# Kernel tuning notes

Hardware: AMD Instinct MI355X
Metric: run time of the kernel (lower is better)

The kernel has to match this reference:

```python
import jax, jax.numpy as jnp
import numpy as np

N = 20000      # nodes
E = 200000     # edges
IN = 128       # in_feat
OUT = 128      # out_feat
NB = 8         # num_bases
SI = IN // NB  # submat_in = 16
SO = OUT // NB # submat_out = 16
R = 230        # num_rels
T = 365        # total_times


def setup_inputs() -> dict:
    key = jax.random.key(0)
    ks = jax.random.split(key, 11)
    h = jax.random.normal(ks[0], (N, IN), jnp.float32)
    edge_norm = jax.random.uniform(ks[1], (E, 1), jnp.float32)
    node_norm = jax.random.uniform(ks[2], (N, 1), jnp.float32)
    weight = jax.random.normal(ks[3], (R, NB * SI * SO), jnp.float32) * 0.05
    h_bias = jnp.zeros((OUT,), jnp.float32)
    loop_weight = jax.random.normal(ks[4], (IN, OUT), jnp.float32) * 0.05
    time_embed = jax.random.normal(ks[5], (T, IN), jnp.float32) * 0.05
    edge_src = jax.random.randint(ks[6], (E,), 0, N)
    edge_dst = jax.random.randint(ks[7], (E,), 0, N)
    edge_type = jax.random.randint(ks[8], (E,), 0, R)
    time_idx = jax.random.randint(ks[9], (N,), 0, T)
    return dict(h=h, edge_norm=edge_norm, node_norm=node_norm, weight=weight,
                h_bias=h_bias, loop_weight=loop_weight, time_embed=time_embed,
                edge_src=edge_src, edge_dst=edge_dst, edge_type=edge_type,
                time_idx=time_idx)


def reference(h, edge_norm, node_norm, weight, h_bias, loop_weight, time_embed,
              edge_src, edge_dst, edge_type, time_idx):
    # self-loop message
    loop_message = h @ loop_weight                              # [N, OUT]
    # msg_func: per-edge relation weight gather + block-diagonal bmm
    W_e = weight[edge_type].reshape(-1, NB, SI, SO)             # [E, NB, SI, SO]
    src = h[edge_src].reshape(-1, NB, SI)                       # [E, NB, SI]
    msg = jnp.einsum('ebi,ebio->ebo', src, W_e).reshape(-1, OUT)  # [E, OUT]
    msg = msg * edge_norm
    # fn.sum aggregation over destination nodes
    agg = jax.ops.segment_sum(msg, edge_dst, num_segments=N)    # [N, OUT]
    # apply_func: scale by node norm, then bias + self loop + activation
    node_repr = agg * node_norm
    node_repr = node_repr + h_bias + loop_message
    node_repr = jax.nn.relu(node_repr)
    # get_time_embedding: per-node time embedding gather
    time_embedding = time_embed[time_idx]                       # [N, IN]
    return node_repr, time_embedding
```

## Files before the change

### kernel.cpp

```cpp
#include <hip/hip_runtime.h>

#define N 20000
#define E 200000
#define IN 128
#define OUT 128
#define NB 8
#define SI 16
#define SO 16
#define R 230
#define T 365

#define NSH 8
#define NSEG (R * NSH)

#define ALLOC_BLOCKS 86
#define SL_BLOCKS 625
#define TE_BLOCKS 313
#define GRID2 (ALLOC_BLOCKS + SL_BLOCKS + TE_BLOCKS)

__device__ float  g_W_t[(size_t)R * NB * SO * SI];
__device__ ushort g_msg[(size_t)E * OUT];
__device__ float  g_sl[(size_t)N * OUT];
__device__ int    g_cnt_d[N];
__device__ int    g_off_d[N];
__device__ int    g_cur_d[N];
__device__ int    g_cnt_r[NSEG * 16];
__device__ int    g_cur_r[NSEG * 16];
__device__ int    g_eid_r[E];
__device__ int    g_total_d;
__device__ int    g_total_r;

__device__ __forceinline__ ushort f2bf(float f) {
    unsigned u = __float_as_uint(f);
    return (ushort)((u + 0x7fffu + ((u >> 16) & 1u)) >> 16);
}
__device__ __forceinline__ float bflo(unsigned m) { return __uint_as_float(m << 16); }
__device__ __forceinline__ float bfhi(unsigned m) { return __uint_as_float(m & 0xffff0000u); }

__global__ __launch_bounds__(256) void hist_kernel(
        const float* __restrict__ weight,
        const int* __restrict__ edge_dst,
        const int* __restrict__ edge_type) {
    __shared__ int lh[NSEG];
    const int tid  = threadIdx.x;
    const int gtid = blockIdx.x * 256 + tid;
    const int GSZ  = gridDim.x * 256;

    for (int t = gtid; t < R * NB * SI * SO; t += GSZ) {
        int r  = t >> 11;
        int b  = (t >> 8) & 7;
        int ol = (t >> 4) & 15;
        int i  = t & 15;
        g_W_t[t] = weight[(size_t)r * 2048 + b * 256 + i * 16 + ol];
    }
    for (int j = tid; j < NSEG; j += 256) lh[j] = 0;
    __syncthreads();
    for (int e = gtid; e < E; e += GSZ) {
        atomicAdd(&g_cnt_d[edge_dst[e]], 1);
        atomicAdd(&lh[edge_type[e] * NSH + (e & (NSH - 1))], 1);
    }
    __syncthreads();
    for (int j = tid; j < NSEG; j += 256)
        if (lh[j]) atomicAdd(&g_cnt_r[j * 16], lh[j]);
}

__global__ __launch_bounds__(256) void alloc_aux_kernel(
        const float* __restrict__ h,
        const float* __restrict__ loop_weight,
        const float* __restrict__ h_bias,
        const float* __restrict__ time_embed,
        const int* __restrict__ time_idx,
        float* __restrict__ out) {
    __shared__ __attribute__((aligned(16))) float hsm[32 * 132];
    const int bid = blockIdx.x;
    const int tid = threadIdx.x;

    if (bid < ALLOC_BLOCKS) {
        const int idx  = bid * 256 + tid;
        const int lane = tid & 63;
        const int NPAD = 20032;
        if (idx < NPAD) {
            int c = (idx < N) ? g_cnt_d[idx] : 0;
            int x = c;
            for (int d = 1; d < 64; d <<= 1) {
                int y = __shfl_up(x, d);
                if (lane >= d) x += y;
            }
            int base = 0;
            if (lane == 63) base = atomicAdd(&g_total_d, x);
            base = __shfl(base, 63);
            if (idx < N) {
                int off = base + x - c;
                g_off_d[idx] = off;
                g_cur_d[idx] = off;
            }
        } else {
            int j = idx - NPAD;
            if (j < 1856) {
                int c = (j < NSEG) ? g_cnt_r[j * 16] : 0;
                int x = c;
                for (int d = 1; d < 64; d <<= 1) {
                    int y = __shfl_up(x, d);
                    if (lane >= d) x += y;
                }
                int base = 0;
                if (lane == 63) base = atomicAdd(&g_total_r, x);
                base = __shfl(base, 63);
                if (j < NSEG) g_cur_r[j * 16] = base + x - c;
            }
        }
        return;
    }

    if (bid < ALLOC_BLOCKS + SL_BLOCKS) {
        const int a   = bid - ALLOC_BLOCKS;
        const int nb0 = a * 32;

        for (int k = tid; k < 32 * IN; k += 256) {
            int nl = k >> 7;
            int i  = k & 127;
            hsm[nl * 132 + i] = h[(size_t)(nb0 + nl) * IN + i];
        }
        __syncthreads();

        const int q    = tid & 63;
        const int wave = tid >> 6;
        const int nb   = wave * 8;
        const float2* lw2 = reinterpret_cast<const float2*>(loop_weight);
        float sL[8], sH[8];
#pragma unroll
        for (int j = 0; j < 8; ++j) { sL[j] = 0.f; sH[j] = 0.f; }
        for (int i0 = 0; i0 < IN; i0 += 4) {
            float2 w0 = lw2[(size_t)(i0 + 0) * 64 + q];
            float2 w1 = lw2[(size_t)(i0 + 1) * 64 + q];
            float2 w2 = lw2[(size_t)(i0 + 2) * 64 + q];
            float2 w3 = lw2[(size_t)(i0 + 3) * 64 + q];
#pragma unroll
            for (int j = 0; j < 8; ++j) {
                float4 v = *reinterpret_cast<const float4*>(
                    &hsm[(nb + j) * 132 + i0]);
                sL[j] = fmaf(v.x, w0.x, sL[j]); sL[j] = fmaf(v.y, w1.x, sL[j]);
                sL[j] = fmaf(v.z, w2.x, sL[j]); sL[j] = fmaf(v.w, w3.x, sL[j]);
                sH[j] = fmaf(v.x, w0.y, sH[j]); sH[j] = fmaf(v.y, w1.y, sH[j]);
                sH[j] = fmaf(v.z, w2.y, sH[j]); sH[j] = fmaf(v.w, w3.y, sH[j]);
            }
        }
        const float2 bias = reinterpret_cast<const float2*>(h_bias)[q];
        float2* sl2 = reinterpret_cast<float2*>(g_sl);
#pragma unroll
        for (int j = 0; j < 8; ++j) {
            float2 v; v.x = sL[j] + bias.x; v.y = sH[j] + bias.y;
            sl2[(size_t)(nb0 + nb + j) * 64 + q] = v;
        }
        return;
    }

    const int c    = bid - ALLOC_BLOCKS - SL_BLOCKS;
    const int row  = tid >> 2;
    const int part = tid & 3;
    const int n    = c * 64 + row;
    if (n < N) {
        const float4* src = reinterpret_cast<const float4*>(
            time_embed + (size_t)time_idx[n] * IN);
        float4* dst = reinterpret_cast<float4*>(
            out + (size_t)N * OUT + (size_t)n * IN);
#pragma unroll
        for (int j = 0; j < 8; ++j)
            dst[part * 8 + j] = src[part * 8 + j];
    }
}

__global__ void scatter_kernel(const int* __restrict__ edge_type) {
    int e = blockIdx.x * blockDim.x + threadIdx.x;
    if (e < E) {
        int seg = edge_type[e] * NSH + (e & (NSH - 1));
        int pr = atomicAdd(&g_cur_r[seg * 16], 1);
        g_eid_r[pr] = e;
    }
}

__global__ __launch_bounds__(256) void msg_kernel(
        const float* __restrict__ h,
        const float* __restrict__ edge_norm,
        const int* __restrict__ edge_src,
        const int* __restrict__ edge_dst,
        const int* __restrict__ edge_type) {
    __shared__ __attribute__((aligned(16))) float hsm[32 * 132];
    __shared__ int   ssrc[32], stype[32], spos[32];
    __shared__ float snorm[32];

    const int tid = threadIdx.x;
    const int lo  = blockIdx.x * 32;

    if (tid < 32) {
        int e = g_eid_r[lo + tid];
        ssrc[tid]  = edge_src[e];
        stype[tid] = edge_type[e];
        snorm[tid] = edge_norm[e];
        spos[tid]  = atomicAdd(&g_cur_d[edge_dst[e]], 1);
    }
    __syncthreads();

    {
        const int row = tid >> 3;
        const int c0  = (tid & 7) * 4;
        const float* hp = h + (size_t)ssrc[row] * IN;
        float* dst = &hsm[row * 132];
#pragma unroll
        for (int j = 0; j < 4; ++j) {
            float4 v = *reinterpret_cast<const float4*>(hp + c0 + 32 * j);
            *reinterpret_cast<float4*>(dst + c0 + 32 * j) = v;
        }
    }
    __syncthreads();

    const int slot = tid >> 7;
    const int o    = tid & 127;
    const int b    = o >> 4;
    const int ol   = o & 15;

#define MSG_BODY(K, W0, W1, W2, W3)                                          \
    {                                                                        \
        const float* hrow = &hsm[(K) * 132 + b * 16];                        \
        float4 h0 = *reinterpret_cast<const float4*>(hrow);                  \
        float4 h1 = *reinterpret_cast<const float4*>(hrow + 4);              \
        float4 h2 = *reinterpret_cast<const float4*>(hrow + 8);              \
        float4 h3 = *reinterpret_cast<const float4*>(hrow + 12);             \
        float m0 = 0.f, m1 = 0.f;                                            \
        m0 = fmaf(h0.x, W0.x, m0); m0 = fmaf(h0.y, W0.y, m0);                \
        m0 = fmaf(h0.z, W0.z, m0); m0 = fmaf(h0.w, W0.w, m0);                \
        m1 = fmaf(h1.x, W1.x, m1); m1 = fmaf(h1.y, W1.y, m1);                \
        m1 = fmaf(h1.z, W1.z, m1); m1 = fmaf(h1.w, W1.w, m1);                \
        m0 = fmaf(h2.x, W2.x, m0); m0 = fmaf(h2.y, W2.y, m0);                \
        m0 = fmaf(h2.z, W2.z, m0); m0 = fmaf(h2.w, W2.w, m0);                \
        m1 = fmaf(h3.x, W3.x, m1); m1 = fmaf(h3.y, W3.y, m1);                \
        m1 = fmaf(h3.z, W3.z, m1); m1 = fmaf(h3.w, W3.w, m1);                \
        __builtin_nontemporal_store(f2bf(snorm[K] * (m0 + m1)),              \
                                    &g_msg[(size_t)spos[K] * OUT + o]);      \
    }

    if (stype[0] == stype[31]) {
        const float4* wp = reinterpret_cast<const float4*>(
            g_W_t + (size_t)stype[0] * 2048 + b * 256 + ol * 16);
        float4 w0 = wp[0], w1 = wp[1], w2 = wp[2], w3 = wp[3];
#pragma unroll 4
        for (int k = slot; k < 32; k += 2)
            MSG_BODY(k, w0, w1, w2, w3)
    } else {
        int rcur = -1;
        float4 w0, w1, w2, w3;
        for (int k = slot; k < 32; k += 2) {
            int r = stype[k];
            if (r != rcur) {
                const float4* wp = reinterpret_cast<const float4*>(
                    g_W_t + (size_t)r * 2048 + b * 256 + ol * 16);
                w0 = wp[0]; w1 = wp[1]; w2 = wp[2]; w3 = wp[3];
                rcur = r;
            }
            MSG_BODY(k, w0, w1, w2, w3)
        }
    }
#undef MSG_BODY
}

__global__ __launch_bounds__(256) void node_kernel(
        const float* __restrict__ node_norm,
        float* __restrict__ out) {
    const int t    = threadIdx.x;
    const int q    = t & 63;
    const int wave = t >> 6;
    const int base = blockIdx.x * 16 + wave * 4;

    const unsigned* msg32 = reinterpret_cast<const unsigned*>(g_msg);
    const float2*   sl2   = reinterpret_cast<const float2*>(g_sl);
    float2*         o2    = reinterpret_cast<float2*>(out);

#pragma unroll
    for (int nl = 0; nl < 4; ++nl) {
        const int n  = base + nl;
        const int st = g_off_d[n];
        const int cn = g_cnt_d[n];
        const unsigned* mp = msg32 + (size_t)st * 64 + q;
        float aL0 = 0.f, aL1 = 0.f, aH0 = 0.f, aH1 = 0.f;
        int k = 0;
        for (; k + 3 < cn; k += 4) {
            unsigned m0 = __builtin_nontemporal_load(mp + (size_t)(k + 0) * 64);
            unsigned m1 = __builtin_nontemporal_load(mp + (size_t)(k + 1) * 64);
            unsigned m2 = __builtin_nontemporal_load(mp + (size_t)(k + 2) * 64);
            unsigned m3 = __builtin_nontemporal_load(mp + (size_t)(k + 3) * 64);
            aL0 += bflo(m0); aH0 += bfhi(m0);
            aL1 += bflo(m1); aH1 += bfhi(m1);
            aL0 += bflo(m2); aH0 += bfhi(m2);
            aL1 += bflo(m3); aH1 += bfhi(m3);
        }
        for (; k < cn; ++k) {
            unsigned m = __builtin_nontemporal_load(mp + (size_t)k * 64);
            aL0 += bflo(m); aH0 += bfhi(m);
        }
        const float nn = node_norm[n];
        const float2 sl = sl2[(size_t)n * 64 + q];
        float2 v;
        v.x = fmaxf((aL0 + aL1) * nn + sl.x, 0.f);
        v.y = fmaxf((aH0 + aH1) * nn + sl.y, 0.f);
        o2[(size_t)n * 64 + q] = v;
    }

    __syncthreads();
    if (t < 16) g_cnt_d[blockIdx.x * 16 + t] = 0;
    {
        int j = blockIdx.x * 256 + t;
        if (j < NSEG * 16) g_cnt_r[j] = 0;
    }
    if (blockIdx.x == 0 && t == 0) { g_total_d = 0; g_total_r = 0; }
}

extern "C" void kernel_launch(void* const* d_in, const int* in_sizes, int n_in,
                              void* d_out, int out_size, void* d_ws, size_t ws_size,
                              hipStream_t stream) {
    const float* h           = (const float*)d_in[0];
    const float* edge_norm   = (const float*)d_in[1];
    const float* node_norm   = (const float*)d_in[2];
    const float* weight      = (const float*)d_in[3];
    const float* h_bias      = (const float*)d_in[4];
    const float* loop_weight = (const float*)d_in[5];
    const float* time_embed  = (const float*)d_in[6];
    const int*   edge_src    = (const int*)d_in[7];
    const int*   edge_dst    = (const int*)d_in[8];
    const int*   edge_type   = (const int*)d_in[9];
    const int*   time_idx    = (const int*)d_in[10];
    float* out = (float*)d_out;

    hist_kernel<<<400, 256, 0, stream>>>(weight, edge_dst, edge_type);
    alloc_aux_kernel<<<GRID2, 256, 0, stream>>>(h, loop_weight, h_bias,
                                                time_embed, time_idx, out);
    scatter_kernel<<<(E + 255) / 256, 256, 0, stream>>>(edge_type);
    msg_kernel<<<E / 32, 256, 0, stream>>>(h, edge_norm, edge_src,
                                           edge_dst, edge_type);
    node_kernel<<<N / 16, 256, 0, stream>>>(node_norm, out);
}
```

Measured before the change: 199.4 us.

## Fold relation-offset scan into hist, merge scatter into combo, gather bf16 h

The last hist block, picked with a done counter and fences, now computes the relation-segment prefix scan. That lets the edge scatter run inside the combined aux kernel, which removes one kernel launch. hist also converts h to a bf16 copy, so msg_kernel gathers half the bytes per source row. The cost is an extra full pass over h and the bf16 rounding of source features, which adds precision error.

```diff
diff --git a/kernel.cpp b/kernel.cpp
--- a/kernel.cpp
+++ b/kernel.cpp
@@ -13,12 +13,14 @@
 #define NSH 8
 #define NSEG (R * NSH)
 
-#define ALLOC_BLOCKS 86
+#define DA_BLOCKS 86
+#define SC_BLOCKS 782
 #define SL_BLOCKS 625
 #define TE_BLOCKS 313
-#define GRID2 (ALLOC_BLOCKS + SL_BLOCKS + TE_BLOCKS)
+#define GRID2 (DA_BLOCKS + SC_BLOCKS + SL_BLOCKS + TE_BLOCKS)
 
 __device__ float  g_W_t[(size_t)R * NB * SO * SI];
+__device__ __attribute__((aligned(16))) ushort g_hb[(size_t)N * IN];
 __device__ ushort g_msg[(size_t)E * OUT];
 __device__ float  g_sl[(size_t)N * OUT];
 __device__ int    g_cnt_d[N];
@@ -28,7 +30,7 @@
 __device__ int    g_cur_r[NSEG * 16];
 __device__ int    g_eid_r[E];
 __device__ int    g_total_d;
-__device__ int    g_total_r;
+__device__ unsigned g_done;
 
 __device__ __forceinline__ ushort f2bf(float f) {
     unsigned u = __float_as_uint(f);
@@ -36,12 +38,18 @@
 }
 __device__ __forceinline__ float bflo(unsigned m) { return __uint_as_float(m << 16); }
 __device__ __forceinline__ float bfhi(unsigned m) { return __uint_as_float(m & 0xffff0000u); }
+__device__ __forceinline__ int ld_agent(const int* p) {
+    return __hip_atomic_load(p, __ATOMIC_RELAXED, __HIP_MEMORY_SCOPE_AGENT);
+}
 
 __global__ __launch_bounds__(256) void hist_kernel(
         const float* __restrict__ weight,
+        const float* __restrict__ h,
         const int* __restrict__ edge_dst,
         const int* __restrict__ edge_type) {
     __shared__ int lh[NSEG];
+    __shared__ int sscan[256];
+    __shared__ int s_last;
     const int tid  = threadIdx.x;
     const int gtid = blockIdx.x * 256 + tid;
     const int GSZ  = gridDim.x * 256;
@@ -53,6 +61,16 @@
         int i  = t & 15;
         g_W_t[t] = weight[(size_t)r * 2048 + b * 256 + i * 16 + ol];
     }
+    {
+        const float4* h4 = reinterpret_cast<const float4*>(h);
+        ushort4* hb4 = reinterpret_cast<ushort4*>(g_hb);
+        for (int t = gtid; t < N * IN / 4; t += GSZ) {
+            float4 v = h4[t];
+            ushort4 o;
+            o.x = f2bf(v.x); o.y = f2bf(v.y); o.z = f2bf(v.z); o.w = f2bf(v.w);
+            hb4[t] = o;
+        }
+    }
     for (int j = tid; j < NSEG; j += 256) lh[j] = 0;
     __syncthreads();
     for (int e = gtid; e < E; e += GSZ) {
@@ -62,24 +80,60 @@
     __syncthreads();
     for (int j = tid; j < NSEG; j += 256)
         if (lh[j]) atomicAdd(&g_cnt_r[j * 16], lh[j]);
-}
-
-__global__ __launch_bounds__(256) void alloc_aux_kernel(
+
+    __syncthreads();
+    if (tid == 0) {
+        __threadfence();
+        unsigned d = atomicAdd(&g_done, 1u);
+        s_last = (d == (unsigned)(gridDim.x - 1)) ? 1 : 0;
+    }
+    __syncthreads();
+    if (!s_last) return;
+    __threadfence();
+
+    int c[8];
+    const int j0 = tid * 8;
+#pragma unroll
+    for (int u = 0; u < 8; ++u) {
+        int j = j0 + u;
+        c[u] = (j < NSEG) ? ld_agent(&g_cnt_r[j * 16]) : 0;
+    }
+    int s = 0;
+#pragma unroll
+    for (int u = 0; u < 8; ++u) s += c[u];
+    sscan[tid] = s;
+    __syncthreads();
+    for (int d = 1; d < 256; d <<= 1) {
+        int v = (tid >= d) ? sscan[tid - d] : 0;
+        __syncthreads();
+        sscan[tid] += v;
+        __syncthreads();
+    }
+    int run = (tid > 0) ? sscan[tid - 1] : 0;
+#pragma unroll
+    for (int u = 0; u < 8; ++u) {
+        int j = j0 + u;
+        if (j < NSEG) g_cur_r[j * 16] = run;
+        run += c[u];
+    }
+}
+
+__global__ __launch_bounds__(256) void combo_kernel(
         const float* __restrict__ h,
         const float* __restrict__ loop_weight,
         const float* __restrict__ h_bias,
         const float* __restrict__ time_embed,
         const int* __restrict__ time_idx,
+        const int* __restrict__ edge_type,
         float* __restrict__ out) {
     __shared__ __attribute__((aligned(16))) float hsm[32 * 132];
     const int bid = blockIdx.x;
     const int tid = threadIdx.x;
 
-    if (bid < ALLOC_BLOCKS) {
+    if (bid < DA_BLOCKS) {
         const int idx  = bid * 256 + tid;
         const int lane = tid & 63;
-        const int NPAD = 20032;
-        if (idx < NPAD) {
+        if (idx < 20032) {
             int c = (idx < N) ? g_cnt_d[idx] : 0;
             int x = c;
             for (int d = 1; d < 64; d <<= 1) {
@@ -94,26 +148,22 @@
                 g_off_d[idx] = off;
                 g_cur_d[idx] = off;
             }
-        } else {
-            int j = idx - NPAD;
-            if (j < 1856) {
-                int c = (j < NSEG) ? g_cnt_r[j * 16] : 0;
-                int x = c;
-                for (int d = 1; d < 64; d <<= 1) {
-                    int y = __shfl_up(x, d);
-                    if (lane >= d) x += y;
-                }
-                int base = 0;
-                if (lane == 63) base = atomicAdd(&g_total_r, x);
-                base = __shfl(base, 63);
-                if (j < NSEG) g_cur_r[j * 16] = base + x - c;
-            }
         }
         return;
     }
 
-    if (bid < ALLOC_BLOCKS + SL_BLOCKS) {
-        const int a   = bid - ALLOC_BLOCKS;
+    if (bid < DA_BLOCKS + SC_BLOCKS) {
+        int e = (bid - DA_BLOCKS) * 256 + tid;
+        if (e < E) {
+            int seg = edge_type[e] * NSH + (e & (NSH - 1));
+            int pr = atomicAdd(&g_cur_r[seg * 16], 1);
+            g_eid_r[pr] = e;
+        }
+        return;
+    }
+
+    if (bid < DA_BLOCKS + SC_BLOCKS + SL_BLOCKS) {
+        const int a   = bid - DA_BLOCKS - SC_BLOCKS;
         const int nb0 = a * 32;
 
         for (int k = tid; k < 32 * IN; k += 256) {
@@ -155,7 +205,7 @@
         return;
     }
 
-    const int c    = bid - ALLOC_BLOCKS - SL_BLOCKS;
+    const int c    = bid - DA_BLOCKS - SC_BLOCKS - SL_BLOCKS;
     const int row  = tid >> 2;
     const int part = tid & 3;
     const int n    = c * 64 + row;
@@ -170,17 +220,7 @@
     }
 }
 
-__global__ void scatter_kernel(const int* __restrict__ edge_type) {
-    int e = blockIdx.x * blockDim.x + threadIdx.x;
-    if (e < E) {
-        int seg = edge_type[e] * NSH + (e & (NSH - 1));
-        int pr = atomicAdd(&g_cur_r[seg * 16], 1);
-        g_eid_r[pr] = e;
-    }
-}
-
 __global__ __launch_bounds__(256) void msg_kernel(
-        const float* __restrict__ h,
         const float* __restrict__ edge_norm,
         const int* __restrict__ edge_src,
         const int* __restrict__ edge_dst,
@@ -203,14 +243,20 @@
 
     {
         const int row = tid >> 3;
-        const int c0  = (tid & 7) * 4;
-        const float* hp = h + (size_t)ssrc[row] * IN;
-        float* dst = &hsm[row * 132];
-#pragma unroll
-        for (int j = 0; j < 4; ++j) {
-            float4 v = *reinterpret_cast<const float4*>(hp + c0 + 32 * j);
-            *reinterpret_cast<float4*>(dst + c0 + 32 * j) = v;
-        }
+        const int c0  = (tid & 7) * 16;
+        const uint4* hp = reinterpret_cast<const uint4*>(
+            g_hb + (size_t)ssrc[row] * IN + c0);
+        float* dst = &hsm[row * 132 + c0];
+        uint4 a = hp[0], b4 = hp[1];
+        float4 f0, f1, f2, f3;
+        f0.x = bflo(a.x);  f0.y = bfhi(a.x);  f0.z = bflo(a.y);  f0.w = bfhi(a.y);
+        f1.x = bflo(a.z);  f1.y = bfhi(a.z);  f1.z = bflo(a.w);  f1.w = bfhi(a.w);
+        f2.x = bflo(b4.x); f2.y = bfhi(b4.x); f2.z = bflo(b4.y); f2.w = bfhi(b4.y);
+        f3.x = bflo(b4.z); f3.y = bfhi(b4.z); f3.z = bflo(b4.w); f3.w = bfhi(b4.w);
+        *reinterpret_cast<float4*>(dst + 0)  = f0;
+        *reinterpret_cast<float4*>(dst + 4)  = f1;
+        *reinterpret_cast<float4*>(dst + 8)  = f2;
+        *reinterpret_cast<float4*>(dst + 12) = f3;
     }
     __syncthreads();
 
@@ -311,7 +357,7 @@
         int j = blockIdx.x * 256 + t;
         if (j < NSEG * 16) g_cnt_r[j] = 0;
     }
-    if (blockIdx.x == 0 && t == 0) { g_total_d = 0; g_total_r = 0; }
+    if (blockIdx.x == 0 && t == 0) { g_total_d = 0; g_done = 0u; }
 }
 
 extern "C" void kernel_launch(void* const* d_in, const int* in_sizes, int n_in,
@@ -330,11 +376,11 @@
     const int*   time_idx    = (const int*)d_in[10];
     float* out = (float*)d_out;
 
-    hist_kernel<<<400, 256, 0, stream>>>(weight, edge_dst, edge_type);
-    alloc_aux_kernel<<<GRID2, 256, 0, stream>>>(h, loop_weight, h_bias,
-                                                time_embed, time_idx, out);
-    scatter_kernel<<<(E + 255) / 256, 256, 0, stream>>>(edge_type);
-    msg_kernel<<<E / 32, 256, 0, stream>>>(h, edge_norm, edge_src,
+    hist_kernel<<<400, 256, 0, stream>>>(weight, h, edge_dst, edge_type);
+    combo_kernel<<<GRID2, 256, 0, stream>>>(h, loop_weight, h_bias,
+                                            time_embed, time_idx,
+                                            edge_type, out);
+    msg_kernel<<<E / 32, 256, 0, stream>>>(edge_norm, edge_src,
                                            edge_dst, edge_type);
     node_kernel<<<N / 16, 256, 0, stream>>>(node_norm, out);
 }
```

New measurement: 199.7 us. Within noise of the previous version (+0.1%).
